# Kernel optimization log

Measured on AMD Instinct MI355X. Metric: run time of the kernel, lower is better.

The kernel has to match this reference:

```python
import jax, jax.numpy as jnp
import numpy as np

LN_EPS = 1e-5


def _ln(x, g, b):
    m = x.mean(-1, keepdims=True)
    v = ((x - m) ** 2).mean(-1, keepdims=True)
    return (x - m) * jax.lax.rsqrt(v + LN_EPS) * g + b


def _shift(x):
    # token shift: previous timestep, zeros at t=0. x: [B,T,C]
    return jnp.pad(x[:, :-1], ((0, 0), (1, 0), (0, 0)))


def _wkv(time_decay, time_first, k, v):
    # numerically-stable RWKV-v4 WKV scan. k, v: [B,T,C]
    B, T, C = k.shape
    decay = -jnp.exp(time_decay)  # [C], negative per-channel log-decay
    kT = jnp.transpose(k, (1, 0, 2))
    vT = jnp.transpose(v, (1, 0, 2))

    def step(carry, kv):
        aa, bb, pp = carry
        kt, vt = kv
        ww = time_first + kt
        p = jnp.maximum(pp, ww)
        e1 = jnp.exp(pp - p)
        e2 = jnp.exp(ww - p)
        out = (e1 * aa + e2 * vt) / (e1 * bb + e2)
        ww2 = pp + decay
        p2 = jnp.maximum(ww2, kt)
        f1 = jnp.exp(ww2 - p2)
        f2 = jnp.exp(kt - p2)
        return (f1 * aa + f2 * vt, f1 * bb + f2, p2), out

    init = (jnp.zeros((B, C), k.dtype), jnp.zeros((B, C), k.dtype),
            jnp.full((B, C), -1e38, k.dtype))
    _, out = jax.lax.scan(step, init, (kT, vT))
    return jnp.transpose(out, (1, 0, 2))


def setup_inputs() -> dict:
    key = jax.random.key(0)
    ks = jax.random.split(key, 24)
    B, T, Dv, Di = 32, 512, 512, 256
    F = Dv + Di
    H = 4 * F
    n = jax.random.normal
    u = jax.random.uniform(ks[4], (B, T, F, 2), minval=1e-6, maxval=1.0 - 1e-6)
    gumbel = -jnp.log(-jnp.log(u))
    sF = 1.0 / np.sqrt(F).astype(np.float32)
    sH = 1.0 / np.sqrt(H).astype(np.float32)
    return {
        'fv': n(ks[0], (B, T, Dv)),
        'fi': n(ks[1], (B, T, Di)),
        'fuse_W': n(ks[2], (F, 2 * F)) * sF,
        'fuse_b': jnp.zeros((2 * F,)),
        'gumbel': gumbel,
        'ln1_g': jnp.ones((F,)), 'ln1_b': jnp.zeros((F,)),
        'mix_k': jax.random.uniform(ks[5], (F,)),
        'mix_v': jax.random.uniform(ks[6], (F,)),
        'mix_r': jax.random.uniform(ks[7], (F,)),
        'time_decay': n(ks[8], (F,)) * 0.1 - 1.0,
        'time_first': n(ks[9], (F,)) * 0.1,
        'Wk': n(ks[10], (F, F)) * sF,
        'Wv': n(ks[11], (F, F)) * sF,
        'Wr': n(ks[12], (F, F)) * sF,
        'Wo': n(ks[13], (F, F)) * sF,
        'ln2_g': jnp.ones((F,)), 'ln2_b': jnp.zeros((F,)),
        'cmix_k': jax.random.uniform(ks[14], (F,)),
        'cmix_r': jax.random.uniform(ks[15], (F,)),
        'cWk': n(ks[16], (F, H)) * sF,
        'cWv': n(ks[17], (H, F)) * sH,
        'cWr': n(ks[18], (F, F)) * sF,
        'reg_W1': n(ks[19], (F, 128)) * sF,
        'reg_b1': jnp.zeros((128,)),
        'reg_W2': n(ks[20], (128, 6)) / np.sqrt(128).astype(np.float32),
        'reg_b2': jnp.zeros((6,)),
    }


def reference(fv, fi, fuse_W, fuse_b, gumbel, ln1_g, ln1_b, mix_k, mix_v, mix_r,
              time_decay, time_first, Wk, Wv, Wr, Wo, ln2_g, ln2_b,
              cmix_k, cmix_r, cWk, cWv, cWr, reg_W1, reg_b1, reg_W2, reg_b2):
    B, T, _ = fv.shape
    # ---- Fusion_module ('hard'): linear -> gumbel-softmax(hard, tau=1) gating
    feat = jnp.concatenate([fv, fi], axis=-1)            # [B,T,F]
    F = feat.shape[-1]
    logits = (feat @ fuse_W + fuse_b).reshape(B, T, F, 2)
    y = jax.nn.softmax(logits + gumbel, axis=-1)          # tau = 1
    hard = jax.nn.one_hot(jnp.argmax(y, -1), 2, dtype=y.dtype)
    mask = hard + y - jax.lax.stop_gradient(y)            # straight-through
    x = feat * mask[..., 0]

    # ---- RWKV block: time-mixing (WKV scan)
    xn = _ln(x, ln1_g, ln1_b)
    xs = _shift(xn)
    xk = xn * mix_k + xs * (1.0 - mix_k)
    xv = xn * mix_v + xs * (1.0 - mix_v)
    xr = xn * mix_r + xs * (1.0 - mix_r)
    k = xk @ Wk
    v = xv @ Wv
    r = jax.nn.sigmoid(xr @ Wr)
    x = x + (r * _wkv(time_decay, time_first, k, v)) @ Wo

    # ---- RWKV block: channel-mixing
    xn = _ln(x, ln2_g, ln2_b)
    xs = _shift(xn)
    xk = xn * cmix_k + xs * (1.0 - cmix_k)
    xr = xn * cmix_r + xs * (1.0 - cmix_r)
    kk = jnp.square(jax.nn.relu(xk @ cWk))
    x = x + jax.nn.sigmoid(xr @ cWr) * (kk @ cWv)

    h = x @ reg_W1 + reg_b1
    h = jnp.where(h > 0, h, 0.1 * h)
    return h @ reg_W2 + reg_b2                            # [B,T,6]
```

## Files before the change

kernel.cpp:

```cpp
#include <hip/hip_runtime.h>
#include <hip/hip_bf16.h>

#define BT 16384
#define FDIM 768
#define HDIM 3072

typedef __attribute__((ext_vector_type(8))) short bf16x8;
typedef __attribute__((ext_vector_type(4))) float f32x4;
typedef __attribute__((ext_vector_type(4))) int i32x4;
typedef __attribute__((ext_vector_type(2))) float f32x2;

__device__ inline float b2f(unsigned short u) {
  union { unsigned int i; float f; } x; x.i = ((unsigned int)u) << 16; return x.f;
}

__global__ void wconv_kernel(const float* __restrict__ in, __hip_bfloat16* __restrict__ out,
                             int K, int N) {
  __shared__ float tile[32][33];
  int kb = blockIdx.x * 32, nb = blockIdx.y * 32;
  int tx = threadIdx.x & 31, ty = threadIdx.x >> 5;
#pragma unroll
  for (int i = 0; i < 4; ++i) {
    int k = ty + i * 8;
    tile[k][tx] = in[(size_t)(kb + k) * N + nb + tx];
  }
  __syncthreads();
#pragma unroll
  for (int i = 0; i < 4; ++i) {
    int n = ty + i * 8;
    out[(size_t)(nb + n) * K + kb + tx] = __float2bfloat16(tile[tx][n]);
  }
}

__global__ void wdsplit_kernel(const float* __restrict__ W, __hip_bfloat16* __restrict__ out) {
  __shared__ float tile[32][33];
  int kb = blockIdx.x * 32, nb = blockIdx.y * 32;
  int tx = threadIdx.x & 31, ty = threadIdx.x >> 5;
#pragma unroll
  for (int i = 0; i < 4; ++i) {
    int k = ty + i * 8;
    f32x2 p = ((const f32x2*)(W + (size_t)(kb + k) * 1536))[nb + tx];
    tile[k][tx] = p.x - p.y;
  }
  __syncthreads();
#pragma unroll
  for (int i = 0; i < 4; ++i) {
    int n = ty + i * 8;
    float d = tile[tx][n];
    __hip_bfloat16 h1 = __float2bfloat16(d);
    float r1 = d - __bfloat162float(h1);
    __hip_bfloat16 h2 = __float2bfloat16(r1);
    float r2 = r1 - __bfloat162float(h2);
    __hip_bfloat16 h3 = __float2bfloat16(r2);
    size_t base = (size_t)(nb + n) * 2304 + kb + tx;
    out[base] = h1; out[base + 768] = h2; out[base + 1536] = h3;
  }
}

__global__ void featsplit_kernel(const float* __restrict__ fv, const float* __restrict__ fi,
                                 __hip_bfloat16* __restrict__ FS) {
  int idx = blockIdx.x * 256 + threadIdx.x;
  int m = idx / 768, c = idx - m * 768;
  float f = (c < 512) ? fv[(size_t)m * 512 + c] : fi[(size_t)m * 256 + c - 512];
  __hip_bfloat16 h1 = __float2bfloat16(f);
  float r1 = f - __bfloat162float(h1);
  __hip_bfloat16 h2 = __float2bfloat16(r1);
  float r2 = r1 - __bfloat162float(h2);
  __hip_bfloat16 h3 = __float2bfloat16(r2);
  size_t base = (size_t)m * 2304 + c;
  FS[base] = h1; FS[base + 768] = h2; FS[base + 1536] = h3;
}

__global__ void ln_kernel(const float* __restrict__ X, const float* __restrict__ g,
                          const float* __restrict__ b, float* __restrict__ XN) {
  int tok = blockIdx.x * 4 + (threadIdx.x >> 6);
  int lane = threadIdx.x & 63;
  const float* row = X + (size_t)tok * 768;
  float v[12]; float s = 0.f, s2 = 0.f;
#pragma unroll
  for (int i = 0; i < 12; ++i) { float x = row[lane + i * 64]; v[i] = x; s += x; s2 += x * x; }
#pragma unroll
  for (int o = 32; o; o >>= 1) { s += __shfl_xor(s, o); s2 += __shfl_xor(s2, o); }
  float m = s * (1.0f / 768.0f);
  float var = s2 * (1.0f / 768.0f) - m * m;
  float inv = 1.0f / sqrtf(var + 1e-5f);
  float* outr = XN + (size_t)tok * 768;
#pragma unroll
  for (int i = 0; i < 12; ++i) { int c = lane + i * 64; outr[c] = (v[i] - m) * inv * g[c] + b[c]; }
}

__global__ void mix3_kernel(const float* __restrict__ XN, const float* __restrict__ mk,
                            const float* __restrict__ mv, const float* __restrict__ mr,
                            __hip_bfloat16* __restrict__ AK, __hip_bfloat16* __restrict__ AV,
                            __hip_bfloat16* __restrict__ AR) {
  int idx = blockIdx.x * 256 + threadIdx.x;
  int m = idx / 768, c = idx - m * 768;
  float xn = XN[idx];
  float xs = (m & 511) ? XN[idx - 768] : 0.0f;
  float k = mk[c], v = mv[c], r = mr[c];
  AK[idx] = __float2bfloat16(xn * k + xs * (1.0f - k));
  AV[idx] = __float2bfloat16(xn * v + xs * (1.0f - v));
  AR[idx] = __float2bfloat16(xn * r + xs * (1.0f - r));
}

__global__ void mix2_kernel(const float* __restrict__ XN, const float* __restrict__ mk,
                            const float* __restrict__ mr,
                            __hip_bfloat16* __restrict__ AK, __hip_bfloat16* __restrict__ AR) {
  int idx = blockIdx.x * 256 + threadIdx.x;
  int m = idx / 768, c = idx - m * 768;
  float xn = XN[idx];
  float xs = (m & 511) ? XN[idx - 768] : 0.0f;
  float k = mk[c], r = mr[c];
  AK[idx] = __float2bfloat16(xn * k + xs * (1.0f - k));
  AR[idx] = __float2bfloat16(xn * r + xs * (1.0f - r));
}

__global__ void wkv_kernel(const float* __restrict__ K, const float* __restrict__ V,
                           const float* __restrict__ RP, const float* __restrict__ td,
                           const float* __restrict__ tfirst, __hip_bfloat16* __restrict__ RA) {
  int idx = blockIdx.x * 256 + threadIdx.x;
  int b = idx / 768, c = idx - b * 768;
  float decay = -__expf(td[c]);
  float u = tfirst[c];
  float aa = 0.f, bb = 0.f, pp = -1e38f;
  size_t o = (size_t)b * 512 * 768 + c;
  for (int t = 0; t < 512; ++t, o += 768) {
    float kt = K[o], vt = V[o];
    float ww = u + kt;
    float p = fmaxf(pp, ww);
    float e1 = __expf(pp - p), e2 = __expf(ww - p);
    float wkv = (e1 * aa + e2 * vt) / (e1 * bb + e2);
    float ww2 = pp + decay;
    float p2 = fmaxf(ww2, kt);
    float f1 = __expf(ww2 - p2), f2 = __expf(kt - p2);
    aa = f1 * aa + f2 * vt; bb = f1 * bb + f2; pp = p2;
    float r = 1.0f / (1.0f + __expf(-RP[o]));
    RA[o] = __float2bfloat16(r * wkv);
  }
}

__global__ void xcvt_kernel(const float* __restrict__ X, __hip_bfloat16* __restrict__ O) {
  int idx = blockIdx.x * 256 + threadIdx.x;
  O[idx] = __float2bfloat16(X[idx]);
}

__global__ void reg2_kernel(const __hip_bfloat16* __restrict__ Hb, const float* __restrict__ W2,
                            const float* __restrict__ b2, float* __restrict__ out) {
  __shared__ float w[768];
  for (int i = threadIdx.x; i < 768; i += 256) w[i] = W2[i];
  __syncthreads();
  int m = blockIdx.x * 256 + threadIdx.x;
  float acc[6];
#pragma unroll
  for (int j = 0; j < 6; ++j) acc[j] = b2[j];
  const bf16x8* hr8 = (const bf16x8*)(Hb + (size_t)m * 128);
#pragma unroll
  for (int h8 = 0; h8 < 16; ++h8) {
    bf16x8 pk = hr8[h8];
#pragma unroll
    for (int e = 0; e < 8; ++e) {
      float hv = b2f((unsigned short)pk[e]);
      int h = h8 * 8 + e;
#pragma unroll
      for (int j = 0; j < 6; ++j) acc[j] += hv * w[h * 6 + j];
    }
  }
#pragma unroll
  for (int j = 0; j < 6; ++j) out[(size_t)m * 6 + j] = acc[j];
}

enum { EP_NONE = 0, EP_GATE, EP_RESID, EP_RELUSQ, EP_SIGRESID, EP_LEAKY };

template<int EP, bool SPLIT6>
__global__ void gemm_bt(const __hip_bfloat16* __restrict__ A, const __hip_bfloat16* __restrict__ Bt,
                        int M, int N, int Kphys, int Klog,
                        float* __restrict__ outF, __hip_bfloat16* __restrict__ outH,
                        const float* __restrict__ x0, const float* __restrict__ x1,
                        const float* __restrict__ x2, const float* __restrict__ x3) {
  __shared__ __align__(16) unsigned short sA[128 * 64];
  __shared__ __align__(16) unsigned short sB[128 * 64];
  const int tid = threadIdx.x;
  const int lane = tid & 63;
  const int wid = tid >> 6;
  const int tm = blockIdx.x * 128, tn = blockIdx.y * 128;
  const int wr = (wid >> 1) * 64, wc = (wid & 1) * 64;
  const int r16 = lane & 15, kg = lane >> 4;

  f32x4 acc[4][4];
  f32x4 zero = {0.f, 0.f, 0.f, 0.f};
#pragma unroll
  for (int i = 0; i < 4; ++i)
#pragma unroll
    for (int j = 0; j < 4; ++j) acc[i][j] = zero;

  int kbS[4], dstS[4];
  size_t rowOffA[4], rowOffB[4];
#pragma unroll
  for (int i = 0; i < 4; ++i) {
    int ch = tid + i * 256;
    int row = ch >> 3;
    int kb16 = ch & 7;
    kbS[i] = kb16 * 8;
    dstS[i] = row * 128 + ((kb16 * 16) ^ ((row & 7) << 4));
    rowOffA[i] = (size_t)(tm + row) * Kphys;
    rowOffB[i] = (size_t)(tn + row) * Kphys;
  }
  const int ca0 = ((kg ^ (r16 & 7)) << 4);
  const int ca1 = (((4 | kg) ^ (r16 & 7)) << 4);
  const int arow = (wr + r16) * 128;
  const int brow = (wc + r16) * 128;

  const int nsteps = Klog / 64;
  for (int st = 0; st < nsteps; ++st) {
    int k0 = st * 64;
    int kA, kB2;
    if (SPLIT6) {
      static constexpr int mapA[6] = {0, 0, 0, 1, 1, 2};
      static constexpr int mapB[6] = {0, 1, 2, 0, 1, 0};
      int s = k0 / 768; int kr = k0 - s * 768;
      kA = mapA[s] * 768 + kr; kB2 = mapB[s] * 768 + kr;
    } else { kA = k0; kB2 = k0; }
    i32x4 va[4], vb[4];
#pragma unroll
    for (int i = 0; i < 4; ++i) {
      va[i] = *(const i32x4*)(A + rowOffA[i] + kA + kbS[i]);
      vb[i] = *(const i32x4*)(Bt + rowOffB[i] + kB2 + kbS[i]);
    }
#pragma unroll
    for (int i = 0; i < 4; ++i) {
      *(i32x4*)((char*)sA + dstS[i]) = va[i];
      *(i32x4*)((char*)sB + dstS[i]) = vb[i];
    }
    __syncthreads();
#pragma unroll
    for (int ks = 0; ks < 2; ++ks) {
      const int ca = ks ? ca1 : ca0;
      bf16x8 af[4], bfv[4];
#pragma unroll
      for (int f = 0; f < 4; ++f) {
        af[f]  = *(const bf16x8*)((const char*)sA + arow + f * 2048 + ca);
        bfv[f] = *(const bf16x8*)((const char*)sB + brow + f * 2048 + ca);
      }
#pragma unroll
      for (int fm = 0; fm < 4; ++fm)
#pragma unroll
        for (int fn = 0; fn < 4; ++fn)
          acc[fm][fn] = __builtin_amdgcn_mfma_f32_16x16x32_bf16(af[fm], bfv[fn], acc[fm][fn], 0, 0, 0);
    }
    __syncthreads();
  }

  const int er0 = tm + wr + (lane >> 4) * 4;
  const int ec0 = tn + wc + (lane & 15);
#pragma unroll
  for (int fm = 0; fm < 4; ++fm) {
#pragma unroll
    for (int fn = 0; fn < 4; ++fn) {
#pragma unroll
      for (int j = 0; j < 4; ++j) {
        int row = er0 + fm * 16 + j;
        int col = ec0 + fn * 16;
        float v = acc[fm][fn][j];
        size_t o = (size_t)row * N + col;
        if (EP == EP_NONE) {
          outF[o] = v;
        } else if (EP == EP_RESID) {
          outF[o] += v;
        } else if (EP == EP_GATE) {
          size_t gi = ((size_t)row * 768 + col) * 2;
          float gd = x0[gi] - x0[gi + 1];
          float bd = x3[2 * col] - x3[2 * col + 1];
          float s = v + bd + gd;
          float feat = (col < 512) ? x1[(size_t)row * 512 + col]
                                   : x2[(size_t)row * 256 + col - 512];
          outF[o] = (s >= 0.0f) ? feat : 0.0f;
        } else if (EP == EP_RELUSQ) {
          float r = v > 0.f ? v : 0.f;
          outH[o] = __float2bfloat16(r * r);
        } else if (EP == EP_SIGRESID) {
          float sg = 1.0f / (1.0f + __expf(-x0[o]));
          outF[o] += sg * v;
        } else if (EP == EP_LEAKY) {
          float h = v + x0[col];
          h = h > 0.f ? h : 0.1f * h;
          outH[o] = __float2bfloat16(h);
        }
      }
    }
  }
}

extern "C" void kernel_launch(void* const* d_in, const int* in_sizes, int n_in,
                              void* d_out, int out_size, void* d_ws, size_t ws_size,
                              hipStream_t stream) {
  const float* fv     = (const float*)d_in[0];
  const float* fi     = (const float*)d_in[1];
  const float* fuse_W = (const float*)d_in[2];
  const float* fuse_b = (const float*)d_in[3];
  const float* gumbel = (const float*)d_in[4];
  const float* ln1_g  = (const float*)d_in[5];
  const float* ln1_b  = (const float*)d_in[6];
  const float* mix_k  = (const float*)d_in[7];
  const float* mix_v  = (const float*)d_in[8];
  const float* mix_r  = (const float*)d_in[9];
  const float* td     = (const float*)d_in[10];
  const float* tfirst = (const float*)d_in[11];
  const float* Wk     = (const float*)d_in[12];
  const float* Wv     = (const float*)d_in[13];
  const float* Wr     = (const float*)d_in[14];
  const float* Wo     = (const float*)d_in[15];
  const float* ln2_g  = (const float*)d_in[16];
  const float* ln2_b  = (const float*)d_in[17];
  const float* cmk    = (const float*)d_in[18];
  const float* cmr    = (const float*)d_in[19];
  const float* cWk    = (const float*)d_in[20];
  const float* cWv    = (const float*)d_in[21];
  const float* cWr    = (const float*)d_in[22];
  const float* rW1    = (const float*)d_in[23];
  const float* rb1    = (const float*)d_in[24];
  const float* rW2    = (const float*)d_in[25];
  const float* rb2    = (const float*)d_in[26];

  char* ws = (char*)d_ws;
  float* X  = (float*)(ws + 0);
  float* XN = (float*)(ws + 50331648UL);
  float* Kb = (float*)(ws + 100663296UL);
  float* Vb = (float*)(ws + 150994944UL);
  float* RP = (float*)(ws + 201326592UL);
  __hip_bfloat16* AK  = (__hip_bfloat16*)(ws + 251658240UL);
  __hip_bfloat16* AV  = (__hip_bfloat16*)(ws + 276824064UL);
  __hip_bfloat16* AR  = (__hip_bfloat16*)(ws + 301989888UL);
  __hip_bfloat16* RA  = (__hip_bfloat16*)(ws + 327155712UL);
  __hip_bfloat16* Hb  = (__hip_bfloat16*)(ws + 352321536UL);
  __hip_bfloat16* WdT = (__hip_bfloat16*)(ws + 356515840UL);
  __hip_bfloat16* WkT = (__hip_bfloat16*)(ws + 360054784UL);
  __hip_bfloat16* WvT = (__hip_bfloat16*)(ws + 361234432UL);
  __hip_bfloat16* WrT = (__hip_bfloat16*)(ws + 362414080UL);
  __hip_bfloat16* WoT = (__hip_bfloat16*)(ws + 363593728UL);
  __hip_bfloat16* cWkT = (__hip_bfloat16*)(ws + 364773376UL);
  __hip_bfloat16* cWvT = (__hip_bfloat16*)(ws + 369491968UL);
  __hip_bfloat16* cWrT = (__hip_bfloat16*)(ws + 374210560UL);
  __hip_bfloat16* W1T  = (__hip_bfloat16*)(ws + 375390208UL);
  __hip_bfloat16* FS = (__hip_bfloat16*)(ws + 100663296UL);
  __hip_bfloat16* KK = (__hip_bfloat16*)(ws + 100663296UL);

  dim3 blk(256);

  wconv_kernel<<<dim3(24, 24), blk, 0, stream>>>(Wk, WkT, 768, 768);
  wconv_kernel<<<dim3(24, 24), blk, 0, stream>>>(Wv, WvT, 768, 768);
  wconv_kernel<<<dim3(24, 24), blk, 0, stream>>>(Wr, WrT, 768, 768);
  wconv_kernel<<<dim3(24, 24), blk, 0, stream>>>(Wo, WoT, 768, 768);
  wconv_kernel<<<dim3(24, 96), blk, 0, stream>>>(cWk, cWkT, 768, 3072);
  wconv_kernel<<<dim3(96, 24), blk, 0, stream>>>(cWv, cWvT, 3072, 768);
  wconv_kernel<<<dim3(24, 24), blk, 0, stream>>>(cWr, cWrT, 768, 768);
  wconv_kernel<<<dim3(24, 4),  blk, 0, stream>>>(rW1, W1T, 768, 128);
  wdsplit_kernel<<<dim3(24, 24), blk, 0, stream>>>(fuse_W, WdT);

  featsplit_kernel<<<49152, blk, 0, stream>>>(fv, fi, FS);
  gemm_bt<EP_GATE, true><<<dim3(128, 6), blk, 0, stream>>>(
      FS, WdT, BT, 768, 2304, 4608, X, nullptr, gumbel, fv, fi, fuse_b);

  ln_kernel<<<4096, blk, 0, stream>>>(X, ln1_g, ln1_b, XN);
  mix3_kernel<<<49152, blk, 0, stream>>>(XN, mix_k, mix_v, mix_r, AK, AV, AR);
  gemm_bt<EP_NONE, false><<<dim3(128, 6), blk, 0, stream>>>(
      AK, WkT, BT, 768, 768, 768, Kb, nullptr, nullptr, nullptr, nullptr, nullptr);
  gemm_bt<EP_NONE, false><<<dim3(128, 6), blk, 0, stream>>>(
      AV, WvT, BT, 768, 768, 768, Vb, nullptr, nullptr, nullptr, nullptr, nullptr);
  gemm_bt<EP_NONE, false><<<dim3(128, 6), blk, 0, stream>>>(
      AR, WrT, BT, 768, 768, 768, RP, nullptr, nullptr, nullptr, nullptr, nullptr);
  wkv_kernel<<<96, blk, 0, stream>>>(Kb, Vb, RP, td, tfirst, RA);
  gemm_bt<EP_RESID, false><<<dim3(128, 6), blk, 0, stream>>>(
      RA, WoT, BT, 768, 768, 768, X, nullptr, nullptr, nullptr, nullptr, nullptr);

  ln_kernel<<<4096, blk, 0, stream>>>(X, ln2_g, ln2_b, XN);
  mix2_kernel<<<49152, blk, 0, stream>>>(XN, cmk, cmr, AK, AR);
  gemm_bt<EP_RELUSQ, false><<<dim3(128, 24), blk, 0, stream>>>(
      AK, cWkT, BT, 3072, 768, 768, nullptr, KK, nullptr, nullptr, nullptr, nullptr);
  gemm_bt<EP_NONE, false><<<dim3(128, 6), blk, 0, stream>>>(
      AR, cWrT, BT, 768, 768, 768, RP, nullptr, nullptr, nullptr, nullptr, nullptr);
  gemm_bt<EP_SIGRESID, false><<<dim3(128, 6), blk, 0, stream>>>(
      KK, cWvT, BT, 768, 3072, 3072, X, nullptr, RP, nullptr, nullptr, nullptr);

  xcvt_kernel<<<49152, blk, 0, stream>>>(X, AV);
  gemm_bt<EP_LEAKY, false><<<dim3(128, 1), blk, 0, stream>>>(
      AV, W1T, BT, 128, 768, 768, nullptr, Hb, rb1, nullptr, nullptr, nullptr);
  reg2_kernel<<<64, blk, 0, stream>>>(Hb, rW2, rb2, (float*)d_out);
}
```

Measured before the change: 1.141 ms.

## Fuse LN with token-shift mixing, batch QKV GEMMs, use LDS direct loads

Several changes land together. LayerNorm is fused with the token-shift mix kernels, the K/V/R projections run as one batched GEMM launch over blockIdx.z, and the final residual epilogue writes bf16 directly so the separate conversion kernel goes away. The GEMM now stages tiles with global_load_lds straight into shared memory instead of going through registers. Feature splitting is vectorised, the WKV scan prefetches the next four timesteps, and five weight conversions share one launch. The aim is fewer launches, less fp32 round-trip traffic and better GEMM load efficiency, at the cost of extra recomputed LN rows and reliance on the contiguous workspace layout for batching.

```diff
diff --git a/kernel.cpp b/kernel.cpp
--- a/kernel.cpp
+++ b/kernel.cpp
@@ -12,6 +12,39 @@
 
 __device__ inline float b2f(unsigned short u) {
   union { unsigned int i; float f; } x; x.i = ((unsigned int)u) << 16; return x.f;
+}
+
+#define GLOAD16(gptr, lptr)                                                    \
+  __builtin_amdgcn_global_load_lds(                                            \
+      (const __attribute__((address_space(1))) void*)(gptr),                   \
+      (__attribute__((address_space(3))) void*)(lptr), 16, 0, 0)
+
+__global__ void wconv5_kernel(const float* s0, const float* s1, const float* s2,
+                              const float* s3, const float* s4,
+                              __hip_bfloat16* d0, __hip_bfloat16* d1, __hip_bfloat16* d2,
+                              __hip_bfloat16* d3, __hip_bfloat16* d4) {
+  const float* in; __hip_bfloat16* out;
+  switch (blockIdx.z) {
+    case 0: in = s0; out = d0; break;
+    case 1: in = s1; out = d1; break;
+    case 2: in = s2; out = d2; break;
+    case 3: in = s3; out = d3; break;
+    default: in = s4; out = d4; break;
+  }
+  __shared__ float tile[32][33];
+  int kb = blockIdx.x * 32, nb = blockIdx.y * 32;
+  int tx = threadIdx.x & 31, ty = threadIdx.x >> 5;
+#pragma unroll
+  for (int i = 0; i < 4; ++i) {
+    int k = ty + i * 8;
+    tile[k][tx] = in[(size_t)(kb + k) * 768 + nb + tx];
+  }
+  __syncthreads();
+#pragma unroll
+  for (int i = 0; i < 4; ++i) {
+    int n = ty + i * 8;
+    out[(size_t)(nb + n) * 768 + kb + tx] = __float2bfloat16(tile[tx][n]);
+  }
 }
 
 __global__ void wconv_kernel(const float* __restrict__ in, __hip_bfloat16* __restrict__ out,
@@ -59,60 +92,105 @@
 
 __global__ void featsplit_kernel(const float* __restrict__ fv, const float* __restrict__ fi,
                                  __hip_bfloat16* __restrict__ FS) {
-  int idx = blockIdx.x * 256 + threadIdx.x;
-  int m = idx / 768, c = idx - m * 768;
-  float f = (c < 512) ? fv[(size_t)m * 512 + c] : fi[(size_t)m * 256 + c - 512];
-  __hip_bfloat16 h1 = __float2bfloat16(f);
-  float r1 = f - __bfloat162float(h1);
-  __hip_bfloat16 h2 = __float2bfloat16(r1);
-  float r2 = r1 - __bfloat162float(h2);
-  __hip_bfloat16 h3 = __float2bfloat16(r2);
-  size_t base = (size_t)m * 2304 + c;
-  FS[base] = h1; FS[base + 768] = h2; FS[base + 1536] = h3;
-}
-
-__global__ void ln_kernel(const float* __restrict__ X, const float* __restrict__ g,
-                          const float* __restrict__ b, float* __restrict__ XN) {
-  int tok = blockIdx.x * 4 + (threadIdx.x >> 6);
-  int lane = threadIdx.x & 63;
-  const float* row = X + (size_t)tok * 768;
-  float v[12]; float s = 0.f, s2 = 0.f;
-#pragma unroll
-  for (int i = 0; i < 12; ++i) { float x = row[lane + i * 64]; v[i] = x; s += x; s2 += x * x; }
-#pragma unroll
-  for (int o = 32; o; o >>= 1) { s += __shfl_xor(s, o); s2 += __shfl_xor(s2, o); }
-  float m = s * (1.0f / 768.0f);
-  float var = s2 * (1.0f / 768.0f) - m * m;
-  float inv = 1.0f / sqrtf(var + 1e-5f);
-  float* outr = XN + (size_t)tok * 768;
-#pragma unroll
-  for (int i = 0; i < 12; ++i) { int c = lane + i * 64; outr[c] = (v[i] - m) * inv * g[c] + b[c]; }
-}
-
-__global__ void mix3_kernel(const float* __restrict__ XN, const float* __restrict__ mk,
-                            const float* __restrict__ mv, const float* __restrict__ mr,
-                            __hip_bfloat16* __restrict__ AK, __hip_bfloat16* __restrict__ AV,
-                            __hip_bfloat16* __restrict__ AR) {
-  int idx = blockIdx.x * 256 + threadIdx.x;
-  int m = idx / 768, c = idx - m * 768;
-  float xn = XN[idx];
-  float xs = (m & 511) ? XN[idx - 768] : 0.0f;
-  float k = mk[c], v = mv[c], r = mr[c];
-  AK[idx] = __float2bfloat16(xn * k + xs * (1.0f - k));
-  AV[idx] = __float2bfloat16(xn * v + xs * (1.0f - v));
-  AR[idx] = __float2bfloat16(xn * r + xs * (1.0f - r));
-}
-
-__global__ void mix2_kernel(const float* __restrict__ XN, const float* __restrict__ mk,
-                            const float* __restrict__ mr,
-                            __hip_bfloat16* __restrict__ AK, __hip_bfloat16* __restrict__ AR) {
-  int idx = blockIdx.x * 256 + threadIdx.x;
-  int m = idx / 768, c = idx - m * 768;
-  float xn = XN[idx];
-  float xs = (m & 511) ? XN[idx - 768] : 0.0f;
-  float k = mk[c], r = mr[c];
-  AK[idx] = __float2bfloat16(xn * k + xs * (1.0f - k));
-  AR[idx] = __float2bfloat16(xn * r + xs * (1.0f - r));
+  int idx4 = blockIdx.x * 256 + threadIdx.x;
+  int m = idx4 / 192, q = idx4 - m * 192;
+  int c0 = q * 4;
+  f32x4 f;
+  if (c0 < 512) f = *(const f32x4*)(fv + (size_t)m * 512 + c0);
+  else          f = *(const f32x4*)(fi + (size_t)m * 256 + (c0 - 512));
+  unsigned short h1[4], h2[4], h3[4];
+#pragma unroll
+  for (int j = 0; j < 4; ++j) {
+    float x = f[j];
+    __hip_bfloat16 a = __float2bfloat16(x);
+    float r1 = x - __bfloat162float(a);
+    __hip_bfloat16 b = __float2bfloat16(r1);
+    float r2 = r1 - __bfloat162float(b);
+    __hip_bfloat16 c = __float2bfloat16(r2);
+    h1[j] = *(unsigned short*)&a; h2[j] = *(unsigned short*)&b; h3[j] = *(unsigned short*)&c;
+  }
+  size_t base = (size_t)m * 2304 + c0;
+  *(ushort4*)((unsigned short*)FS + base)        = make_ushort4(h1[0], h1[1], h1[2], h1[3]);
+  *(ushort4*)((unsigned short*)FS + base + 768)  = make_ushort4(h2[0], h2[1], h2[2], h2[3]);
+  *(ushort4*)((unsigned short*)FS + base + 1536) = make_ushort4(h3[0], h3[1], h3[2], h3[3]);
+}
+
+__global__ void lnmix3_kernel(const float* __restrict__ X, const float* __restrict__ g,
+                              const float* __restrict__ b, const float* __restrict__ mk,
+                              const float* __restrict__ mv, const float* __restrict__ mr,
+                              __hip_bfloat16* __restrict__ AK, __hip_bfloat16* __restrict__ AV,
+                              __hip_bfloat16* __restrict__ AR) {
+  __shared__ float xn[5][768];
+  int tok0 = blockIdx.x * 4;
+  int w = threadIdx.x >> 6, lane = threadIdx.x & 63;
+  int t = tok0 + w - 1;
+  if (t >= 0) {
+    const float* row = X + (size_t)t * 768;
+    float vv[12]; float s = 0.f, s2 = 0.f;
+#pragma unroll
+    for (int i = 0; i < 12; ++i) { float x = row[lane + i * 64]; vv[i] = x; s += x; s2 += x * x; }
+#pragma unroll
+    for (int o = 32; o; o >>= 1) { s += __shfl_xor(s, o); s2 += __shfl_xor(s2, o); }
+    float m = s * (1.0f / 768.0f);
+    float var = s2 * (1.0f / 768.0f) - m * m;
+    float inv = 1.0f / sqrtf(var + 1e-5f);
+#pragma unroll
+    for (int i = 0; i < 12; ++i) { int c = lane + i * 64; xn[w][c] = (vv[i] - m) * inv * g[c] + b[c]; }
+  }
+  __syncthreads();
+  if (w >= 1) {
+    int tt = tok0 + (w - 1);
+    bool first = (tt & 511) == 0;
+    size_t base = (size_t)tt * 768;
+#pragma unroll
+    for (int i = 0; i < 12; ++i) {
+      int c = lane + i * 64;
+      float a = xn[w][c];
+      float sft = first ? 0.0f : xn[w - 1][c];
+      float k = mk[c], v = mv[c], r = mr[c];
+      AK[base + c] = __float2bfloat16(a * k + sft * (1.0f - k));
+      AV[base + c] = __float2bfloat16(a * v + sft * (1.0f - v));
+      AR[base + c] = __float2bfloat16(a * r + sft * (1.0f - r));
+    }
+  }
+}
+
+__global__ void lnmix2_kernel(const float* __restrict__ X, const float* __restrict__ g,
+                              const float* __restrict__ b, const float* __restrict__ mk,
+                              const float* __restrict__ mr,
+                              __hip_bfloat16* __restrict__ AK, __hip_bfloat16* __restrict__ AR) {
+  __shared__ float xn[5][768];
+  int tok0 = blockIdx.x * 4;
+  int w = threadIdx.x >> 6, lane = threadIdx.x & 63;
+  int t = tok0 + w - 1;
+  if (t >= 0) {
+    const float* row = X + (size_t)t * 768;
+    float vv[12]; float s = 0.f, s2 = 0.f;
+#pragma unroll
+    for (int i = 0; i < 12; ++i) { float x = row[lane + i * 64]; vv[i] = x; s += x; s2 += x * x; }
+#pragma unroll
+    for (int o = 32; o; o >>= 1) { s += __shfl_xor(s, o); s2 += __shfl_xor(s2, o); }
+    float m = s * (1.0f / 768.0f);
+    float var = s2 * (1.0f / 768.0f) - m * m;
+    float inv = 1.0f / sqrtf(var + 1e-5f);
+#pragma unroll
+    for (int i = 0; i < 12; ++i) { int c = lane + i * 64; xn[w][c] = (vv[i] - m) * inv * g[c] + b[c]; }
+  }
+  __syncthreads();
+  if (w >= 1) {
+    int tt = tok0 + (w - 1);
+    bool first = (tt & 511) == 0;
+    size_t base = (size_t)tt * 768;
+#pragma unroll
+    for (int i = 0; i < 12; ++i) {
+      int c = lane + i * 64;
+      float a = xn[w][c];
+      float sft = first ? 0.0f : xn[w - 1][c];
+      float k = mk[c], r = mr[c];
+      AK[base + c] = __float2bfloat16(a * k + sft * (1.0f - k));
+      AR[base + c] = __float2bfloat16(a * r + sft * (1.0f - r));
+    }
+  }
 }
 
 __global__ void wkv_kernel(const float* __restrict__ K, const float* __restrict__ V,
@@ -124,24 +202,35 @@
   float u = tfirst[c];
   float aa = 0.f, bb = 0.f, pp = -1e38f;
   size_t o = (size_t)b * 512 * 768 + c;
-  for (int t = 0; t < 512; ++t, o += 768) {
-    float kt = K[o], vt = V[o];
-    float ww = u + kt;
-    float p = fmaxf(pp, ww);
-    float e1 = __expf(pp - p), e2 = __expf(ww - p);
-    float wkv = (e1 * aa + e2 * vt) / (e1 * bb + e2);
-    float ww2 = pp + decay;
-    float p2 = fmaxf(ww2, kt);
-    float f1 = __expf(ww2 - p2), f2 = __expf(kt - p2);
-    aa = f1 * aa + f2 * vt; bb = f1 * bb + f2; pp = p2;
-    float r = 1.0f / (1.0f + __expf(-RP[o]));
-    RA[o] = __float2bfloat16(r * wkv);
-  }
-}
-
-__global__ void xcvt_kernel(const float* __restrict__ X, __hip_bfloat16* __restrict__ O) {
-  int idx = blockIdx.x * 256 + threadIdx.x;
-  O[idx] = __float2bfloat16(X[idx]);
+  float ck[4], cv[4], cr[4], nk[4], nv[4], nr[4];
+#pragma unroll
+  for (int j = 0; j < 4; ++j) { size_t oj = o + (size_t)j * 768; ck[j] = K[oj]; cv[j] = V[oj]; cr[j] = RP[oj]; }
+  size_t ob = o;
+  for (int g = 0; g < 128; ++g) {
+    size_t onext = (g == 127) ? o : ob + 3072;
+#pragma unroll
+    for (int j = 0; j < 4; ++j) {
+      size_t oj = onext + (size_t)j * 768;
+      nk[j] = K[oj]; nv[j] = V[oj]; nr[j] = RP[oj];
+    }
+#pragma unroll
+    for (int j = 0; j < 4; ++j) {
+      float kt = ck[j], vt = cv[j];
+      float ww = u + kt;
+      float p = fmaxf(pp, ww);
+      float e1 = __expf(pp - p), e2 = __expf(ww - p);
+      float wkv = (e1 * aa + e2 * vt) / (e1 * bb + e2);
+      float ww2 = pp + decay;
+      float p2 = fmaxf(ww2, kt);
+      float f1 = __expf(ww2 - p2), f2 = __expf(kt - p2);
+      aa = f1 * aa + f2 * vt; bb = f1 * bb + f2; pp = p2;
+      float r = 1.0f / (1.0f + __expf(-cr[j]));
+      RA[ob + (size_t)j * 768] = __float2bfloat16(r * wkv);
+    }
+#pragma unroll
+    for (int j = 0; j < 4; ++j) { ck[j] = nk[j]; cv[j] = nv[j]; cr[j] = nr[j]; }
+    ob += 3072;
+  }
 }
 
 __global__ void reg2_kernel(const __hip_bfloat16* __restrict__ Hb, const float* __restrict__ W2,
@@ -173,7 +262,8 @@
 
 template<int EP, bool SPLIT6>
 __global__ void gemm_bt(const __hip_bfloat16* __restrict__ A, const __hip_bfloat16* __restrict__ Bt,
-                        int M, int N, int Kphys, int Klog,
+                        int N, int Kphys, int Klog,
+                        size_t aZ, size_t bZ, size_t oZ,
                         float* __restrict__ outF, __hip_bfloat16* __restrict__ outH,
                         const float* __restrict__ x0, const float* __restrict__ x1,
                         const float* __restrict__ x2, const float* __restrict__ x3) {
@@ -185,6 +275,8 @@
   const int tm = blockIdx.x * 128, tn = blockIdx.y * 128;
   const int wr = (wid >> 1) * 64, wc = (wid & 1) * 64;
   const int r16 = lane & 15, kg = lane >> 4;
+  const int z = blockIdx.z;
+  A += (size_t)z * aZ; Bt += (size_t)z * bZ;
 
   f32x4 acc[4][4];
   f32x4 zero = {0.f, 0.f, 0.f, 0.f};
@@ -193,17 +285,16 @@
 #pragma unroll
     for (int j = 0; j < 4; ++j) acc[i][j] = zero;
 
-  int kbS[4], dstS[4];
-  size_t rowOffA[4], rowOffB[4];
-#pragma unroll
-  for (int i = 0; i < 4; ++i) {
-    int ch = tid + i * 256;
-    int row = ch >> 3;
-    int kb16 = ch & 7;
-    kbS[i] = kb16 * 8;
-    dstS[i] = row * 128 + ((kb16 * 16) ^ ((row & 7) << 4));
-    rowOffA[i] = (size_t)(tm + row) * Kphys;
-    rowOffB[i] = (size_t)(tn + row) * Kphys;
+  size_t gA[4], gB[4];
+  int ldsOff[4];
+#pragma unroll
+  for (int i = 0; i < 4; ++i) {
+    int c = (wid << 2) | i;
+    int row = (c << 3) | (lane >> 3);
+    int swz = ((lane & 7) ^ (row & 7)) << 3;
+    gA[i] = (size_t)(tm + row) * Kphys + swz;
+    gB[i] = (size_t)(tn + row) * Kphys + swz;
+    ldsOff[i] = c << 9;
   }
   const int ca0 = ((kg ^ (r16 & 7)) << 4);
   const int ca1 = (((4 | kg) ^ (r16 & 7)) << 4);
@@ -220,17 +311,10 @@
       int s = k0 / 768; int kr = k0 - s * 768;
       kA = mapA[s] * 768 + kr; kB2 = mapB[s] * 768 + kr;
     } else { kA = k0; kB2 = k0; }
-    i32x4 va[4], vb[4];
-#pragma unroll
-    for (int i = 0; i < 4; ++i) {
-      va[i] = *(const i32x4*)(A + rowOffA[i] + kA + kbS[i]);
-      vb[i] = *(const i32x4*)(Bt + rowOffB[i] + kB2 + kbS[i]);
-    }
-#pragma unroll
-    for (int i = 0; i < 4; ++i) {
-      *(i32x4*)((char*)sA + dstS[i]) = va[i];
-      *(i32x4*)((char*)sB + dstS[i]) = vb[i];
-    }
+#pragma unroll
+    for (int i = 0; i < 4; ++i) GLOAD16(A + gA[i] + kA, sA + ldsOff[i]);
+#pragma unroll
+    for (int i = 0; i < 4; ++i) GLOAD16(Bt + gB[i] + kB2, sB + ldsOff[i]);
     __syncthreads();
 #pragma unroll
     for (int ks = 0; ks < 2; ++ks) {
@@ -263,7 +347,7 @@
         float v = acc[fm][fn][j];
         size_t o = (size_t)row * N + col;
         if (EP == EP_NONE) {
-          outF[o] = v;
+          outF[(size_t)z * oZ + o] = v;
         } else if (EP == EP_RESID) {
           outF[o] += v;
         } else if (EP == EP_GATE) {
@@ -279,7 +363,8 @@
           outH[o] = __float2bfloat16(r * r);
         } else if (EP == EP_SIGRESID) {
           float sg = 1.0f / (1.0f + __expf(-x0[o]));
-          outF[o] += sg * v;
+          float xv = x1[o] + sg * v;
+          outH[o] = __float2bfloat16(xv);
         } else if (EP == EP_LEAKY) {
           float h = v + x0[col];
           h = h > 0.f ? h : 0.1f * h;
@@ -323,9 +408,7 @@
 
   char* ws = (char*)d_ws;
   float* X  = (float*)(ws + 0);
-  float* XN = (float*)(ws + 50331648UL);
   float* Kb = (float*)(ws + 100663296UL);
-  float* Vb = (float*)(ws + 150994944UL);
   float* RP = (float*)(ws + 201326592UL);
   __hip_bfloat16* AK  = (__hip_bfloat16*)(ws + 251658240UL);
   __hip_bfloat16* AV  = (__hip_bfloat16*)(ws + 276824064UL);
@@ -334,55 +417,46 @@
   __hip_bfloat16* Hb  = (__hip_bfloat16*)(ws + 352321536UL);
   __hip_bfloat16* WdT = (__hip_bfloat16*)(ws + 356515840UL);
   __hip_bfloat16* WkT = (__hip_bfloat16*)(ws + 360054784UL);
-  __hip_bfloat16* WvT = (__hip_bfloat16*)(ws + 361234432UL);
-  __hip_bfloat16* WrT = (__hip_bfloat16*)(ws + 362414080UL);
-  __hip_bfloat16* WoT = (__hip_bfloat16*)(ws + 363593728UL);
   __hip_bfloat16* cWkT = (__hip_bfloat16*)(ws + 364773376UL);
   __hip_bfloat16* cWvT = (__hip_bfloat16*)(ws + 369491968UL);
   __hip_bfloat16* cWrT = (__hip_bfloat16*)(ws + 374210560UL);
   __hip_bfloat16* W1T  = (__hip_bfloat16*)(ws + 375390208UL);
+  __hip_bfloat16* WvT = (__hip_bfloat16*)(ws + 361234432UL);
+  __hip_bfloat16* WrT = (__hip_bfloat16*)(ws + 362414080UL);
+  __hip_bfloat16* WoT = (__hip_bfloat16*)(ws + 363593728UL);
   __hip_bfloat16* FS = (__hip_bfloat16*)(ws + 100663296UL);
   __hip_bfloat16* KK = (__hip_bfloat16*)(ws + 100663296UL);
 
   dim3 blk(256);
 
-  wconv_kernel<<<dim3(24, 24), blk, 0, stream>>>(Wk, WkT, 768, 768);
-  wconv_kernel<<<dim3(24, 24), blk, 0, stream>>>(Wv, WvT, 768, 768);
-  wconv_kernel<<<dim3(24, 24), blk, 0, stream>>>(Wr, WrT, 768, 768);
-  wconv_kernel<<<dim3(24, 24), blk, 0, stream>>>(Wo, WoT, 768, 768);
+  wconv5_kernel<<<dim3(24, 24, 5), blk, 0, stream>>>(Wk, Wv, Wr, Wo, cWr,
+                                                     WkT, WvT, WrT, WoT, cWrT);
   wconv_kernel<<<dim3(24, 96), blk, 0, stream>>>(cWk, cWkT, 768, 3072);
   wconv_kernel<<<dim3(96, 24), blk, 0, stream>>>(cWv, cWvT, 3072, 768);
-  wconv_kernel<<<dim3(24, 24), blk, 0, stream>>>(cWr, cWrT, 768, 768);
   wconv_kernel<<<dim3(24, 4),  blk, 0, stream>>>(rW1, W1T, 768, 128);
   wdsplit_kernel<<<dim3(24, 24), blk, 0, stream>>>(fuse_W, WdT);
 
-  featsplit_kernel<<<49152, blk, 0, stream>>>(fv, fi, FS);
-  gemm_bt<EP_GATE, true><<<dim3(128, 6), blk, 0, stream>>>(
-      FS, WdT, BT, 768, 2304, 4608, X, nullptr, gumbel, fv, fi, fuse_b);
-
-  ln_kernel<<<4096, blk, 0, stream>>>(X, ln1_g, ln1_b, XN);
-  mix3_kernel<<<49152, blk, 0, stream>>>(XN, mix_k, mix_v, mix_r, AK, AV, AR);
-  gemm_bt<EP_NONE, false><<<dim3(128, 6), blk, 0, stream>>>(
-      AK, WkT, BT, 768, 768, 768, Kb, nullptr, nullptr, nullptr, nullptr, nullptr);
-  gemm_bt<EP_NONE, false><<<dim3(128, 6), blk, 0, stream>>>(
-      AV, WvT, BT, 768, 768, 768, Vb, nullptr, nullptr, nullptr, nullptr, nullptr);
-  gemm_bt<EP_NONE, false><<<dim3(128, 6), blk, 0, stream>>>(
-      AR, WrT, BT, 768, 768, 768, RP, nullptr, nullptr, nullptr, nullptr, nullptr);
-  wkv_kernel<<<96, blk, 0, stream>>>(Kb, Vb, RP, td, tfirst, RA);
-  gemm_bt<EP_RESID, false><<<dim3(128, 6), blk, 0, stream>>>(
-      RA, WoT, BT, 768, 768, 768, X, nullptr, nullptr, nullptr, nullptr, nullptr);
-
-  ln_kernel<<<4096, blk, 0, stream>>>(X, ln2_g, ln2_b, XN);
-  mix2_kernel<<<49152, blk, 0, stream>>>(XN, cmk, cmr, AK, AR);
-  gemm_bt<EP_RELUSQ, false><<<dim3(128, 24), blk, 0, stream>>>(
-      AK, cWkT, BT, 3072, 768, 768, nullptr, KK, nullptr, nullptr, nullptr, nullptr);
-  gemm_bt<EP_NONE, false><<<dim3(128, 6), blk, 0, stream>>>(
-      AR, cWrT, BT, 768, 768, 768, RP, nullptr, nullptr, nullptr, nullptr, nullptr);
-  gemm_bt<EP_SIGRESID, false><<<dim3(128, 6), blk, 0, stream>>>(
-      KK, cWvT, BT, 768, 3072, 3072, X, nullptr, RP, nullptr, nullptr, nullptr);
-
-  xcvt_kernel<<<49152, blk, 0, stream>>>(X, AV);
-  gemm_bt<EP_LEAKY, false><<<dim3(128, 1), blk, 0, stream>>>(
-      AV, W1T, BT, 128, 768, 768, nullptr, Hb, rb1, nullptr, nullptr, nullptr);
+  featsplit_kernel<<<12288, blk, 0, stream>>>(fv, fi, FS);
+  gemm_bt<EP_GATE, true><<<dim3(128, 6, 1), blk, 0, stream>>>(
+      FS, WdT, 768, 2304, 4608, 0, 0, 0, X, nullptr, gumbel, fv, fi, fuse_b);
+
+  lnmix3_kernel<<<4096, dim3(320), 0, stream>>>(X, ln1_g, ln1_b, mix_k, mix_v, mix_r, AK, AV, AR);
+  gemm_bt<EP_NONE, false><<<dim3(128, 6, 3), blk, 0, stream>>>(
+      AK, WkT, 768, 768, 768, 12582912UL, 589824UL, 12582912UL,
+      Kb, nullptr, nullptr, nullptr, nullptr, nullptr);
+  wkv_kernel<<<96, blk, 0, stream>>>(Kb, Kb + 12582912UL, RP, td, tfirst, RA);
+  gemm_bt<EP_RESID, false><<<dim3(128, 6, 1), blk, 0, stream>>>(
+      RA, WoT, 768, 768, 768, 0, 0, 0, X, nullptr, nullptr, nullptr, nullptr, nullptr);
+
+  lnmix2_kernel<<<4096, dim3(320), 0, stream>>>(X, ln2_g, ln2_b, cmk, cmr, AK, AR);
+  gemm_bt<EP_RELUSQ, false><<<dim3(128, 24, 1), blk, 0, stream>>>(
+      AK, cWkT, 3072, 768, 768, 0, 0, 0, nullptr, KK, nullptr, nullptr, nullptr, nullptr);
+  gemm_bt<EP_NONE, false><<<dim3(128, 6, 1), blk, 0, stream>>>(
+      AR, cWrT, 768, 768, 768, 0, 0, 0, RP, nullptr, nullptr, nullptr, nullptr, nullptr);
+  gemm_bt<EP_SIGRESID, false><<<dim3(128, 6, 1), blk, 0, stream>>>(
+      KK, cWvT, 768, 3072, 3072, 0, 0, 0, nullptr, AV, RP, X, nullptr, nullptr);
+
+  gemm_bt<EP_LEAKY, false><<<dim3(128, 1, 1), blk, 0, stream>>>(
+      AV, W1T, 128, 768, 768, 0, 0, 0, nullptr, Hb, rb1, nullptr, nullptr, nullptr);
   reg2_kernel<<<64, blk, 0, stream>>>(Hb, rW2, rb2, (float*)d_out);
 }
```

Result: faster. 934.0 us (-18.2%).
